# Kernel optimization log

Hardware: AMD Instinct MI355X
Metric: run time of the kernel (lower is better)

The kernel has to match this reference:

```python
import jax, jax.numpy as jnp
import numpy as np

B, S, D, H = 2, 2048, 1024, 16
DH = D // H


def setup_inputs() -> dict:
    key = jax.random.key(0)
    ks = jax.random.split(key, 7)
    scale = 1.0 / np.sqrt(D)
    return {
        "query": jax.random.normal(ks[0], (B, S, D), jnp.float32),
        "key": jax.random.normal(ks[1], (B, S, D), jnp.float32),
        "value": jax.random.normal(ks[2], (B, S, D), jnp.float32),
        # causal mask, broadcast over batch and heads
        "mask": jnp.tril(jnp.ones((S, S), bool))[None, None, :, :],
        "wq": jax.random.normal(ks[3], (D, D), jnp.float32) * scale,
        "wk": jax.random.normal(ks[4], (D, D), jnp.float32) * scale,
        "wv": jax.random.normal(ks[5], (D, D), jnp.float32) * scale,
        "wo": jax.random.normal(ks[6], (D, D), jnp.float32) * scale,
    }


def reference(query, key, value, mask, wq, wk, wv, wo):
    # nn.Linear(bias=False): y = x @ W.T
    def split_heads(x):
        return x.reshape(B, -1, H, DH).transpose(0, 2, 1, 3)  # [B,H,S,DH]

    q = split_heads(query @ wq.T)
    k = split_heads(key @ wk.T)
    v = split_heads(value @ wv.T)

    scores = jnp.einsum("bhqd,bhkd->bhqk", q, k) / jnp.sqrt(jnp.float32(DH))
    scores = jnp.where(mask, scores, jnp.float32(-1e9))
    p_attn = jax.nn.softmax(scores, axis=-1)  # dropout inactive (eval / p=0)
    x = jnp.einsum("bhqk,bhkd->bhqd", p_attn, v)
    x = x.transpose(0, 2, 1, 3).reshape(B, -1, D)
    return x @ wo.T
```

## Files before the change

kernel.cpp:

```cpp
#include <hip/hip_runtime.h>
#include <hip/hip_bf16.h>


typedef __bf16 bf16x8 __attribute__((ext_vector_type(8)));
typedef float f32x4 __attribute__((ext_vector_type(4)));

#define AS1 __attribute__((address_space(1)))
#define AS3 __attribute__((address_space(3)))

__device__ __forceinline__ void load_lds16(const void* g, void* l) {
    __builtin_amdgcn_global_load_lds((const AS1 void*)g, (AS3 void*)l, 16, 0, 0);
}

__global__ __launch_bounds__(256) void cast_many(const float* __restrict__ a0,
                                                 const float* __restrict__ a1,
                                                 const float* __restrict__ a2,
                                                 const float* __restrict__ a3,
                                                 __hip_bfloat16* __restrict__ d,
                                                 size_t per, int n4) {
    const float* s = (blockIdx.y == 0) ? a0 : (blockIdx.y == 1) ? a1 : (blockIdx.y == 2) ? a2 : a3;
    d += (size_t)blockIdx.y * per;
    int i = blockIdx.x * 256 + threadIdx.x;
    if (i >= n4) return;
    float4 v = reinterpret_cast<const float4*>(s)[i];
    union { __hip_bfloat16 h[4]; short4 s4; } u;
    u.h[0] = __float2bfloat16(v.x);
    u.h[1] = __float2bfloat16(v.y);
    u.h[2] = __float2bfloat16(v.z);
    u.h[3] = __float2bfloat16(v.w);
    reinterpret_cast<short4*>(d)[i] = u.s4;
}

template <int BM, int MODE>
__global__ __launch_bounds__(256) void gemm_bt(const __hip_bfloat16* __restrict__ Ab,
                                               const __hip_bfloat16* __restrict__ Wb,
                                               float* __restrict__ Cf,
                                               __hip_bfloat16* __restrict__ Qb,
                                               __hip_bfloat16* __restrict__ Kb,
                                               __hip_bfloat16* __restrict__ Vtb) {
    constexpr int Kn = 1024, BK = 32, MW = BM / 32;
    constexpr size_t MD = (size_t)4096 * 1024;

    __shared__ __hip_bfloat16 sA[BM * BK];
    __shared__ __hip_bfloat16 sB[128 * BK];

    const int t = threadIdx.x, w = t >> 6, l = t & 63;
    const int lr = l & 15, lk = (l >> 4) * 8;
    const int mbase = blockIdx.y * BM, nbase = blockIdx.x * 128;
    const int wr = (w >> 1) * (BM / 2), wc = (w & 1) * 64;

    const __hip_bfloat16* A = Ab;
    if constexpr (MODE == 1) A = Ab + (size_t)(nbase >> 10) * MD;

    f32x4 acc[MW][4] = {};

    for (int k0 = 0; k0 < Kn; k0 += BK) {
#pragma unroll
        for (int i = 0; i < BM / 64; i++) {
            const int c = i * 256 + t;
            load_lds16(&A[(size_t)(mbase + (c >> 2)) * Kn + k0 + (c & 3) * 8],
                       &sA[(i * 256 + w * 64) * 8]);
        }
#pragma unroll
        for (int i = 0; i < 2; i++) {
            const int c = i * 256 + t;
            load_lds16(&Wb[(size_t)(nbase + (c >> 2)) * Kn + k0 + (c & 3) * 8],
                       &sB[(i * 256 + w * 64) * 8]);
        }
        __syncthreads();
        bf16x8 af[MW], bfr[4];
#pragma unroll
        for (int m = 0; m < MW; m++) af[m] = *(const bf16x8*)&sA[(wr + m * 16 + lr) * BK + lk];
#pragma unroll
        for (int n = 0; n < 4; n++) bfr[n] = *(const bf16x8*)&sB[(wc + n * 16 + lr) * BK + lk];
#pragma unroll
        for (int m = 0; m < MW; m++)
#pragma unroll
            for (int n = 0; n < 4; n++)
                acc[m][n] = __builtin_amdgcn_mfma_f32_16x16x32_bf16(af[m], bfr[n], acc[m][n], 0, 0, 0);
        __syncthreads();
    }

    const int row0 = mbase + wr + (l >> 4) * 4;
    if constexpr (MODE == 0) {
#pragma unroll
        for (int m = 0; m < MW; m++)
#pragma unroll
            for (int n = 0; n < 4; n++)
#pragma unroll
                for (int r = 0; r < 4; r++)
                    Cf[(size_t)(row0 + m * 16 + r) * 1024 + nbase + wc + n * 16 + lr] = acc[m][n][r];
    } else {
        const int region = nbase >> 10;
        const int colL = (nbase & 1023) + wc + lr;
        if (region < 2) {
            __hip_bfloat16* Ob = (region == 0) ? Qb : Kb;
            const float alpha = (region == 0) ? 0.125f : 1.0f;
#pragma unroll
            for (int m = 0; m < MW; m++)
#pragma unroll
                for (int n = 0; n < 4; n++)
#pragma unroll
                    for (int r = 0; r < 4; r++)
                        Ob[(size_t)(row0 + m * 16 + r) * 1024 + colL + n * 16] =
                            __float2bfloat16(acc[m][n][r] * alpha);
        } else {
#pragma unroll
            for (int m = 0; m < MW; m++) {
                const int s0 = row0 + m * 16;
                const int b = s0 >> 11, s = s0 & 2047;
#pragma unroll
                for (int n = 0; n < 4; n++) {
                    const int dhg = colL + n * 16;
                    const size_t idx = ((size_t)((b * 16 + (dhg >> 6)) * 64 + (dhg & 63))) * 2048 + s;
                    union { __hip_bfloat16 h[4]; short4 s4; } u;
#pragma unroll
                    for (int r = 0; r < 4; r++) u.h[r] = __float2bfloat16(acc[m][n][r]);
                    *(short4*)&Vtb[idx] = u.s4;
                }
            }
        }
    }
}

__device__ __forceinline__ bf16x8 rd8(const __hip_bfloat16* tile, int row, int colb) {
    return *(const bf16x8*)((const char*)tile + row * 128 + (colb ^ ((row & 7) << 4)));
}

__device__ __forceinline__ void stage_kv(const char* Kg, const char* Vg, void* ksb, void* vsb, int t) {
#pragma unroll
    for (int i = 0; i < 2; i++) {
        const int c = i * 256 + t, row = c >> 3;
        const int colb = ((c & 7) * 16) ^ ((row & 7) << 4);
        load_lds16(Kg + (size_t)row * 2048 + colb, (char*)ksb + (i * 256 + (t & 192)) * 16);
    }
#pragma unroll
    for (int i = 0; i < 2; i++) {
        const int c = i * 256 + t, row = c >> 3;
        const int colb = ((c & 7) * 16) ^ ((row & 7) << 4);
        load_lds16(Vg + (size_t)row * 4096 + colb, (char*)vsb + (i * 256 + (t & 192)) * 16);
    }
}

__global__ __launch_bounds__(256, 4) void attn_causal(const __hip_bfloat16* __restrict__ Qb,
                                                      const __hip_bfloat16* __restrict__ Kb,
                                                      const __hip_bfloat16* __restrict__ Vtb,
                                                      __hip_bfloat16* __restrict__ X) {
    constexpr int S = 2048;
    const int i0 = blockIdx.x;
    const int j = i0 >> 3;
    const int bh = (i0 & 7) * 4 + (j & 3);
    const int qt = 31 - (j >> 2);
    const int b = bh >> 4, h = bh & 15;

    __shared__ __hip_bfloat16 Ks[2][4096];
    __shared__ __hip_bfloat16 Vs[2][4096];
    __shared__ __hip_bfloat16 Pl[4 * 1024];

    const int t = threadIdx.x, w = t >> 6, l = t & 63;
    const int lr = l & 15, lg = l >> 4, lk = lg * 8;

    const __hip_bfloat16* Qbh = Qb + (size_t)b * S * 1024 + h * 64;
    const char* Kbh = (const char*)(Kb + (size_t)b * S * 1024 + h * 64);
    const char* Vbh = (const char*)(Vtb + (size_t)bh * 64 * 2048);
    __hip_bfloat16* Xbh = X + (size_t)b * S * 1024 + h * 64;

    const int qrow = qt * 64 + w * 16;
    bf16x8 qf[2];
#pragma unroll
    for (int kk = 0; kk < 2; kk++)
        qf[kk] = *(const bf16x8*)&Qbh[(size_t)(qrow + lr) * 1024 + kk * 32 + lk];

    f32x4 xacc[4] = {};
    float m = -1e30f, lsum = 0.f;

    stage_kv(Kbh, Vbh, &Ks[0][0], &Vs[0][0], t);

    const int total = qt + 1;
    for (int kt = 0; kt < total; ++kt) {
        if (kt + 1 < total) {
            stage_kv(Kbh + (size_t)((kt + 1) * 64) * 2048, Vbh + (size_t)(kt + 1) * 128,
                     &Ks[(kt + 1) & 1][0], &Vs[(kt + 1) & 1][0], t);
            asm volatile("s_waitcnt vmcnt(4)" ::: "memory");
        } else {
            asm volatile("s_waitcnt vmcnt(0)" ::: "memory");
        }
        __builtin_amdgcn_s_barrier();

        const __hip_bfloat16* Kt = &Ks[kt & 1][0];
        const __hip_bfloat16* Vt = &Vs[kt & 1][0];

        f32x4 sacc[4] = {};
#pragma unroll
        for (int kk = 0; kk < 2; kk++)
#pragma unroll
            for (int n = 0; n < 4; n++)
                sacc[n] = __builtin_amdgcn_mfma_f32_16x16x32_bf16(
                    rd8(Kt, n * 16 + lr, kk * 64 + lg * 16), qf[kk], sacc[n], 0, 0, 0);

        if (kt == qt) {
            const int qg = qrow + lr;
#pragma unroll
            for (int n = 0; n < 4; n++)
#pragma unroll
                for (int r = 0; r < 4; r++)
                    if (kt * 64 + n * 16 + lg * 4 + r > qg) sacc[n][r] = -1e30f;
        }

        float tm = -1e30f;
#pragma unroll
        for (int n = 0; n < 4; n++) {
            float a = fmaxf(fmaxf(sacc[n][0], sacc[n][1]), fmaxf(sacc[n][2], sacc[n][3]));
            tm = fmaxf(tm, a);
        }
        tm = fmaxf(tm, __shfl_xor(tm, 16, 64));
        tm = fmaxf(tm, __shfl_xor(tm, 32, 64));
        const float mn = fmaxf(m, tm);
        const float sc = __expf(m - mn);
        m = mn;
        float pr[4][4], ps = 0.f;
#pragma unroll
        for (int n = 0; n < 4; n++)
#pragma unroll
            for (int r = 0; r < 4; r++) {
                const float pv = __expf(sacc[n][r] - mn);
                pr[n][r] = pv;
                ps += pv;
            }
        ps += __shfl_xor(ps, 16, 64);
        ps += __shfl_xor(ps, 32, 64);
        lsum = lsum * sc + ps;

#pragma unroll
        for (int r = 0; r < 4; r++) {
            const float bsc = __shfl(sc, (lg << 2) + r, 64);
#pragma unroll
            for (int dd = 0; dd < 4; dd++) xacc[dd][r] *= bsc;
        }

#pragma unroll
        for (int n = 0; n < 4; n++) {
            union { __hip_bfloat16 hh[4]; short4 s4; } u;
#pragma unroll
            for (int r = 0; r < 4; r++) u.hh[r] = __float2bfloat16(pr[n][r]);
            *(short4*)((char*)Pl + w * 2048 + lr * 128 +
                       ((n * 32 + lg * 8) ^ ((lr & 7) << 4))) = u.s4;
        }

#pragma unroll
        for (int kk = 0; kk < 2; kk++) {
            const bf16x8 pa = *(const bf16x8*)((const char*)Pl + w * 2048 + lr * 128 +
                                               ((kk * 64 + lg * 16) ^ ((lr & 7) << 4)));
#pragma unroll
            for (int dd = 0; dd < 4; dd++)
                xacc[dd] = __builtin_amdgcn_mfma_f32_16x16x32_bf16(
                    pa, rd8(Vt, dd * 16 + lr, kk * 64 + lg * 16), xacc[dd], 0, 0, 0);
        }
        __builtin_amdgcn_s_barrier();
    }

    const float inv = 1.0f / lsum;
#pragma unroll
    for (int r = 0; r < 4; r++) {
        const float binv = __shfl(inv, (lg << 2) + r, 64);
#pragma unroll
        for (int dd = 0; dd < 4; dd++)
            Xbh[(size_t)(qrow + lg * 4 + r) * 1024 + dd * 16 + lr] =
                __float2bfloat16(xacc[dd][r] * binv);
    }
}

extern "C" void kernel_launch(void* const* d_in, const int* in_sizes, int n_in,
                              void* d_out, int out_size, void* d_ws, size_t ws_size,
                              hipStream_t stream) {
    const float* q_in = (const float*)d_in[0];
    const float* k_in = (const float*)d_in[1];
    const float* v_in = (const float*)d_in[2];
    const float* wq = (const float*)d_in[4];
    const float* wk = (const float*)d_in[5];
    const float* wv = (const float*)d_in[6];
    const float* wo = (const float*)d_in[7];

    const size_t MD = (size_t)4096 * 1024;
    const size_t WD = (size_t)1024 * 1024;

    __hip_bfloat16* ws = (__hip_bfloat16*)d_ws;
    __hip_bfloat16* inb = ws;
    __hip_bfloat16* wb = inb + 3 * MD;
    __hip_bfloat16* Qbuf = wb + 4 * WD;
    __hip_bfloat16* Kbuf = Qbuf + MD;
    __hip_bfloat16* Vtb = Kbuf + MD;
    __hip_bfloat16* xb = Vtb + MD;

    cast_many<<<dim3(4096, 3), 256, 0, stream>>>(q_in, k_in, v_in, q_in, inb, MD, (int)(MD / 4));
    cast_many<<<dim3(1024, 4), 256, 0, stream>>>(wq, wk, wv, wo, wb, WD, (int)(WD / 4));

    gemm_bt<128, 1><<<dim3(24, 32), 256, 0, stream>>>(inb, wb, nullptr, Qbuf, Kbuf, Vtb);

    attn_causal<<<1024, 256, 0, stream>>>(Qbuf, Kbuf, Vtb, xb);

    gemm_bt<64, 0><<<dim3(8, 64), 256, 0, stream>>>(xb, wb + 3 * WD, (float*)d_out,
                                                    nullptr, nullptr, nullptr);
}
```

Measured before the change: 223.1 us.

## Merge cast kernels, fold log2e into Q scale, add lazy rescale and MFMA priority

The two fp32-to-bf16 cast launches become one grid-stride kernel, which removes a launch. The Q scale now includes log2(e), so the softmax can use exp2f instead of __expf. Online-softmax rescaling is skipped unless the tile max exceeds the running max by more than 8 (in log2 units), which cuts shuffles and multiplies on most iterations at some risk of larger unnormalised values. s_setprio is raised around the MFMA blocks to favour matrix issue across waves.

```diff
diff --git a/kernel.cpp b/kernel.cpp
--- a/kernel.cpp
+++ b/kernel.cpp
@@ -12,23 +12,38 @@
     __builtin_amdgcn_global_load_lds((const AS1 void*)g, (AS3 void*)l, 16, 0, 0);
 }
 
-__global__ __launch_bounds__(256) void cast_many(const float* __restrict__ a0,
-                                                 const float* __restrict__ a1,
-                                                 const float* __restrict__ a2,
-                                                 const float* __restrict__ a3,
-                                                 __hip_bfloat16* __restrict__ d,
-                                                 size_t per, int n4) {
-    const float* s = (blockIdx.y == 0) ? a0 : (blockIdx.y == 1) ? a1 : (blockIdx.y == 2) ? a2 : a3;
-    d += (size_t)blockIdx.y * per;
-    int i = blockIdx.x * 256 + threadIdx.x;
-    if (i >= n4) return;
-    float4 v = reinterpret_cast<const float4*>(s)[i];
-    union { __hip_bfloat16 h[4]; short4 s4; } u;
-    u.h[0] = __float2bfloat16(v.x);
-    u.h[1] = __float2bfloat16(v.y);
-    u.h[2] = __float2bfloat16(v.z);
-    u.h[3] = __float2bfloat16(v.w);
-    reinterpret_cast<short4*>(d)[i] = u.s4;
+__global__ __launch_bounds__(256) void cast_all(const float* __restrict__ q,
+                                                const float* __restrict__ k,
+                                                const float* __restrict__ v,
+                                                const float* __restrict__ wq,
+                                                const float* __restrict__ wk,
+                                                const float* __restrict__ wv,
+                                                const float* __restrict__ wo,
+                                                __hip_bfloat16* __restrict__ inb,
+                                                __hip_bfloat16* __restrict__ wb) {
+    const size_t MD = (size_t)4096 * 1024, WD = (size_t)1024 * 1024;
+    const int y = blockIdx.y;
+    const float* s;
+    __hip_bfloat16* d;
+    int n4;
+    if (y < 3) {
+        s = (y == 0) ? q : (y == 1) ? k : v;
+        d = inb + (size_t)y * MD;
+        n4 = (int)(MD / 4);
+    } else {
+        s = (y == 3) ? wq : (y == 4) ? wk : (y == 5) ? wv : wo;
+        d = wb + (size_t)(y - 3) * WD;
+        n4 = (int)(WD / 4);
+    }
+    for (int i = blockIdx.x * 256 + threadIdx.x; i < n4; i += 1024 * 256) {
+        float4 v4 = reinterpret_cast<const float4*>(s)[i];
+        union { __hip_bfloat16 h[4]; short4 s4; } u;
+        u.h[0] = __float2bfloat16(v4.x);
+        u.h[1] = __float2bfloat16(v4.y);
+        u.h[2] = __float2bfloat16(v4.z);
+        u.h[3] = __float2bfloat16(v4.w);
+        reinterpret_cast<short4*>(d)[i] = u.s4;
+    }
 }
 
 template <int BM, int MODE>
@@ -95,7 +110,7 @@
         const int colL = (nbase & 1023) + wc + lr;
         if (region < 2) {
             __hip_bfloat16* Ob = (region == 0) ? Qb : Kb;
-            const float alpha = (region == 0) ? 0.125f : 1.0f;
+            const float alpha = (region == 0) ? 0.18033688011112042f : 1.0f;
 #pragma unroll
             for (int m = 0; m < MW; m++)
 #pragma unroll
@@ -191,12 +206,14 @@
         const __hip_bfloat16* Vt = &Vs[kt & 1][0];
 
         f32x4 sacc[4] = {};
+        __builtin_amdgcn_s_setprio(1);
 #pragma unroll
         for (int kk = 0; kk < 2; kk++)
 #pragma unroll
             for (int n = 0; n < 4; n++)
                 sacc[n] = __builtin_amdgcn_mfma_f32_16x16x32_bf16(
                     rd8(Kt, n * 16 + lr, kk * 64 + lg * 16), qf[kk], sacc[n], 0, 0, 0);
+        __builtin_amdgcn_s_setprio(0);
 
         if (kt == qt) {
             const int qg = qrow + lr;
@@ -207,36 +224,38 @@
                     if (kt * 64 + n * 16 + lg * 4 + r > qg) sacc[n][r] = -1e30f;
         }
 
-        float tm = -1e30f;
-#pragma unroll
-        for (int n = 0; n < 4; n++) {
-            float a = fmaxf(fmaxf(sacc[n][0], sacc[n][1]), fmaxf(sacc[n][2], sacc[n][3]));
-            tm = fmaxf(tm, a);
-        }
+        float tm = fmaxf(fmaxf(sacc[0][0], sacc[0][1]), fmaxf(sacc[0][2], sacc[0][3]));
+#pragma unroll
+        for (int n = 1; n < 4; n++)
+            tm = fmaxf(tm, fmaxf(fmaxf(sacc[n][0], sacc[n][1]), fmaxf(sacc[n][2], sacc[n][3])));
         tm = fmaxf(tm, __shfl_xor(tm, 16, 64));
         tm = fmaxf(tm, __shfl_xor(tm, 32, 64));
-        const float mn = fmaxf(m, tm);
-        const float sc = __expf(m - mn);
-        m = mn;
+
+        if (!__all(tm <= m + 8.0f)) {
+            const float mn = fmaxf(m, tm);
+            const float sc = exp2f(m - mn);
+            m = mn;
+            lsum *= sc;
+#pragma unroll
+            for (int r = 0; r < 4; r++) {
+                const float bsc = __shfl(sc, (lg << 2) + r, 64);
+#pragma unroll
+                for (int dd = 0; dd < 4; dd++) xacc[dd][r] *= bsc;
+            }
+        }
+
         float pr[4][4], ps = 0.f;
 #pragma unroll
         for (int n = 0; n < 4; n++)
 #pragma unroll
             for (int r = 0; r < 4; r++) {
-                const float pv = __expf(sacc[n][r] - mn);
+                const float pv = exp2f(sacc[n][r] - m);
                 pr[n][r] = pv;
                 ps += pv;
             }
         ps += __shfl_xor(ps, 16, 64);
         ps += __shfl_xor(ps, 32, 64);
-        lsum = lsum * sc + ps;
-
-#pragma unroll
-        for (int r = 0; r < 4; r++) {
-            const float bsc = __shfl(sc, (lg << 2) + r, 64);
-#pragma unroll
-            for (int dd = 0; dd < 4; dd++) xacc[dd][r] *= bsc;
-        }
+        lsum += ps;
 
 #pragma unroll
         for (int n = 0; n < 4; n++) {
@@ -247,6 +266,7 @@
                        ((n * 32 + lg * 8) ^ ((lr & 7) << 4))) = u.s4;
         }
 
+        __builtin_amdgcn_s_setprio(1);
 #pragma unroll
         for (int kk = 0; kk < 2; kk++) {
             const bf16x8 pa = *(const bf16x8*)((const char*)Pl + w * 2048 + lr * 128 +
@@ -256,6 +276,7 @@
                 xacc[dd] = __builtin_amdgcn_mfma_f32_16x16x32_bf16(
                     pa, rd8(Vt, dd * 16 + lr, kk * 64 + lg * 16), xacc[dd], 0, 0, 0);
         }
+        __builtin_amdgcn_s_setprio(0);
         __builtin_amdgcn_s_barrier();
     }
 
@@ -292,8 +313,7 @@
     __hip_bfloat16* Vtb = Kbuf + MD;
     __hip_bfloat16* xb = Vtb + MD;
 
-    cast_many<<<dim3(4096, 3), 256, 0, stream>>>(q_in, k_in, v_in, q_in, inb, MD, (int)(MD / 4));
-    cast_many<<<dim3(1024, 4), 256, 0, stream>>>(wq, wk, wv, wo, wb, WD, (int)(WD / 4));
+    cast_all<<<dim3(1024, 7), 256, 0, stream>>>(q_in, k_in, v_in, wq, wk, wv, wo, inb, wb);
 
     gemm_bt<128, 1><<<dim3(24, 32), 256, 0, stream>>>(inb, wb, nullptr, Qbuf, Kbuf, Vtb);
 
```

Measured after the change: 225.2 us. No clear change (+0.9%).
